# Optimization experiments

Measured on AMD Instinct MI355X. Metric: run time of the kernel, lower is better.

Reference implementation:

```python
import jax, jax.numpy as jnp
import numpy as np
import math

N = 50000
E = 500000
IN_C = 128
T_FEAT = 16
OUT_C = 128
EPS = 1e-5
NEG_SLOPE = 0.01


def setup_inputs() -> dict:
    key = jax.random.key(0)
    ks = jax.random.split(key, 10)
    x = jax.random.normal(ks[0], (N, IN_C), dtype=jnp.float32)
    edge_index = jax.random.randint(ks[1], (2, E), 0, N, dtype=jnp.int64)
    edge_weight = jax.random.uniform(ks[2], (E,), dtype=jnp.float32)
    time_diff = jax.random.uniform(ks[3], (1,), dtype=jnp.float32)
    d_in = IN_C + T_FEAT
    morning_freq = jax.random.normal(ks[4], (T_FEAT,), dtype=jnp.float32)
    W_gcn = jax.random.normal(ks[5], (d_in, OUT_C), dtype=jnp.float32) / np.sqrt(d_in)
    b_gcn = jnp.zeros((OUT_C,), dtype=jnp.float32)
    gamma = jnp.ones((OUT_C,), dtype=jnp.float32)
    beta = jnp.zeros((OUT_C,), dtype=jnp.float32)
    W_lin = jax.random.normal(ks[6], (OUT_C, OUT_C), dtype=jnp.float32) / np.sqrt(OUT_C)
    b_lin = jax.random.normal(ks[7], (OUT_C,), dtype=jnp.float32) * 0.01
    return {"x": x, "edge_index": edge_index, "edge_weight": edge_weight,
            "time_diff": time_diff, "morning_freq": morning_freq,
            "W_gcn": W_gcn, "b_gcn": b_gcn, "gamma": gamma, "beta": beta,
            "W_lin": W_lin, "b_lin": b_lin}


def _gcn_conv(h, edge_index, edge_weight):
    # PyG GCNConv aggregation: add self-loops (weight 1), symmetric normalization.
    row, col = edge_index[0], edge_index[1]
    loop = jnp.arange(N, dtype=edge_index.dtype)
    row_f = jnp.concatenate([row, loop])
    col_f = jnp.concatenate([col, loop])
    ew_f = jnp.concatenate([edge_weight, jnp.ones((N,), dtype=h.dtype)])
    deg = jax.ops.segment_sum(ew_f, col_f, num_segments=N)
    dinv = jnp.where(deg > 0, jax.lax.rsqrt(jnp.maximum(deg, 1e-12)), 0.0)
    norm = dinv[row_f] * ew_f * dinv[col_f]                 # [E+N]
    msg = h[row_f] * norm[:, None]                          # gather + scale
    return jax.ops.segment_sum(msg, col_f, num_segments=N)  # scatter-add


def reference(x, edge_index, edge_weight, time_diff, morning_freq,
              W_gcn, b_gcn, gamma, beta, W_lin, b_lin):
    td = time_diff[0]
    # time_segment == 'morning_peak': sin encoding, tiled over all nodes
    enc = jnp.sin(td * morning_freq * math.pi)              # [T]
    enc = jnp.broadcast_to(enc[None, :], (x.shape[0], T_FEAT))
    h = jnp.concatenate([x, enc], axis=1)                   # [N, in+T]
    h = h @ W_gcn                                           # GCN linear transform
    h = _gcn_conv(h, edge_index, edge_weight) + b_gcn       # [N, out]
    # BatchNorm1d (training-mode batch statistics, biased variance)
    mean = jnp.mean(h, axis=0)
    var = jnp.mean(jnp.square(h - mean), axis=0)
    h = gamma * (h - mean) * jax.lax.rsqrt(var + EPS) + beta
    h = jnp.where(h >= 0, h, NEG_SLOPE * h)                 # LeakyReLU
    h = h @ W_lin + b_lin                                   # Linear (dropout=eval identity)
    return h
```

## Files before the change

kernel.cpp:

```cpp
#include <hip/hip_runtime.h>
#include <hip/hip_bf16.h>

#define NN 50000
#define NE 500000
#define C 128
#define NBLK ((NN + 255) / 256)
#define SPB (NN / 8)
#define RB 128
#define RROWS ((SPB + RB - 1) / RB)
#define GB ((NN + 63) / 64)
#define BN_EPS 1e-5f
#define NEG 0.01f
#define WSCALE 16777216.0f
#define WMASK  0xFFFFFFFFFFFULL

typedef __attribute__((ext_vector_type(8))) short bf16x8;
typedef __attribute__((ext_vector_type(4))) float f32x4;

__device__ inline unsigned short f2bf(float f) {
    unsigned int u = __float_as_uint(f);
    unsigned int r = (u + 0x7fffu + ((u >> 16) & 1u)) >> 16;
    return (unsigned short)r;
}
__device__ inline unsigned int pack2(float a, float b) {
    return (unsigned int)f2bf(a) | ((unsigned int)f2bf(b) << 16);
}
__device__ inline float4 bf4_to_f4(uint2 u) {
    float4 r;
    r.x = __uint_as_float(u.x << 16);
    r.y = __uint_as_float(u.x & 0xffff0000u);
    r.z = __uint_as_float(u.y << 16);
    r.w = __uint_as_float(u.y & 0xffff0000u);
    return r;
}

__global__ void zero_kernel(float* __restrict__ p, long n) {
    long i = (long)blockIdx.x * blockDim.x + threadIdx.x;
    long s = (long)gridDim.x * blockDim.x;
    for (; i < n; i += s) p[i] = 0.f;
}

__global__ __launch_bounds__(256) void wprep_kernel(const float* __restrict__ Wg,
                                                    const float* __restrict__ Wl,
                                                    unsigned int* __restrict__ Wgt,
                                                    unsigned int* __restrict__ Wlt) {
    const int t = threadIdx.x;
    const int col = t >> 1;
    const int half = t & 1;
    for (int j = 0; j < 32; j++) {
        int ku = half * 32 + j;
        int k0 = 2 * ku;
        unsigned int g = (unsigned int)((ku >> 2) ^ (col & 15));
        unsigned int slot = (unsigned int)col * 64u + (g << 2) + (unsigned int)(ku & 3);
        Wgt[slot] = pack2(Wg[(size_t)k0 * C + col], Wg[(size_t)(k0 + 1) * C + col]);
        Wlt[slot] = pack2(Wl[(size_t)k0 * C + col], Wl[(size_t)(k0 + 1) * C + col]);
    }
}

__global__ void cvec_kernel(const float* __restrict__ td, const float* __restrict__ mf,
                            const float* __restrict__ Wg, float* __restrict__ cvec) {
    int o = threadIdx.x;
    float t = td[0];
    float acc = 0.f;
#pragma unroll
    for (int j = 0; j < 16; j++) {
        float s = sinf(t * mf[j] * 3.14159265358979323846f);
        acc = fmaf(s, Wg[(128 + j) * C + o], acc);
    }
    cvec[o] = acc;
}

__global__ __launch_bounds__(256) void gemm1_kernel(const float* __restrict__ X,
                                                    const unsigned int* __restrict__ Wt,
                                                    const float* __restrict__ cvec,
                                                    unsigned short* __restrict__ Hb) {
    __shared__ unsigned int wsh[8192];
    const int t = threadIdx.x;
#pragma unroll
    for (int i = 0; i < 8; i++)
        ((uint4*)wsh)[t + i * 256] = ((const uint4*)Wt)[t + i * 256];

    const int lane = t & 63;
    const int wid = t >> 6;
    const int lrow = lane & 15;
    const int kb = lane >> 4;
    const int row = blockIdx.x * 64 + wid * 16 + lrow;
    const float* xrow = X + (size_t)min(row, NN - 1) * C;

    f32x4 acc[8];
#pragma unroll
    for (int n = 0; n < 8; n++) acc[n] = (f32x4){0.f, 0.f, 0.f, 0.f};
    __syncthreads();

#pragma unroll
    for (int ks = 0; ks < 4; ks++) {
        float4 a0 = *(const float4*)(xrow + ks * 32 + kb * 8);
        float4 a1 = *(const float4*)(xrow + ks * 32 + kb * 8 + 4);
        union { unsigned int u[4]; bf16x8 v; } af;
        af.u[0] = pack2(a0.x, a0.y); af.u[1] = pack2(a0.z, a0.w);
        af.u[2] = pack2(a1.x, a1.y); af.u[3] = pack2(a1.z, a1.w);
        const unsigned int gp = (unsigned int)((ks * 4 + kb) ^ lrow);
#pragma unroll
        for (int n = 0; n < 8; n++) {
            int col = n * 16 + lrow;
            union { uint4 q; bf16x8 v; } bfm;
            bfm.q = *(const uint4*)&wsh[col * 64 + gp * 4];
            acc[n] = __builtin_amdgcn_mfma_f32_16x16x32_bf16(af.v, bfm.v, acc[n], 0, 0, 0);
        }
    }
    const int orow = blockIdx.x * 64 + wid * 16 + kb * 4;
#pragma unroll
    for (int n = 0; n < 8; n++) {
        int col = n * 16 + lrow;
        float cv = cvec[col];
#pragma unroll
        for (int i = 0; i < 4; i++) {
            int r = orow + i;
            if (r < NN) Hb[(size_t)r * C + col] = f2bf(acc[n][i] + cv);
        }
    }
}

__global__ void hist_kernel(const int* __restrict__ ei, const float* __restrict__ ew,
                            unsigned long long* __restrict__ hist, int* __restrict__ rank) {
    int e = blockIdx.x * blockDim.x + threadIdx.x;
    if (e < NE) {
        int c = ei[NE + e];
        unsigned long long pack = (1ULL << 44) | (unsigned long long)(ew[e] * WSCALE);
        unsigned long long old = atomicAdd(&hist[c], pack);
        rank[e] = (int)(old >> 44);
    }
}

__global__ __launch_bounds__(256) void scanp1_kernel(const unsigned long long* __restrict__ hist,
                                                     int* __restrict__ rptr,
                                                     int* __restrict__ bsum) {
    __shared__ int s[256];
    const int t = threadIdx.x;
    const int i = blockIdx.x * 256 + t;
    int v = (i < NN) ? (int)(hist[i] >> 44) : 0;
    s[t] = v;
    __syncthreads();
    for (int off = 1; off < 256; off <<= 1) {
        int add = (t >= off) ? s[t - off] : 0;
        __syncthreads();
        s[t] += add;
        __syncthreads();
    }
    if (i < NN) rptr[i] = s[t] - v;
    if (t == 255) bsum[blockIdx.x] = s[255];
}

__global__ __launch_bounds__(256) void scanp2_kernel(const int* __restrict__ bsum,
                                                     int* __restrict__ boff) {
    __shared__ int s[256];
    const int t = threadIdx.x;
    int v = (t < NBLK) ? bsum[t] : 0;
    s[t] = v;
    __syncthreads();
    for (int off = 1; off < 256; off <<= 1) {
        int add = (t >= off) ? s[t - off] : 0;
        __syncthreads();
        s[t] += add;
        __syncthreads();
    }
    if (t < NBLK) boff[t] = s[t] - v;
}

__global__ void scanp3_kernel(int* __restrict__ rptr, const int* __restrict__ boff,
                              const unsigned long long* __restrict__ hist,
                              float* __restrict__ dinv) {
    int i = blockIdx.x * blockDim.x + threadIdx.x;
    if (i < NN) {
        rptr[i] += boff[i >> 8];
        float degw = (float)(hist[i] & WMASK) * (1.0f / WSCALE);
        dinv[i] = rsqrtf(degw + 1.0f);
    }
    if (i == 0) rptr[NN] = NE;
}

__global__ void fill_kernel(const int* __restrict__ ei, const float* __restrict__ ew,
                            const float* __restrict__ dinv, const int* __restrict__ rptr,
                            const int* __restrict__ rank, int2* __restrict__ csr) {
    int e = blockIdx.x * blockDim.x + threadIdx.x;
    if (e >= NE) return;
    int r = ei[e], c = ei[NE + e];
    int slot = rptr[c] + rank[e];
    float w = dinv[r] * ew[e] * dinv[c];
    csr[slot] = make_int2(r, __float_as_int(w));
}

__global__ __launch_bounds__(256) void spmm_kernel(const int* __restrict__ rptr,
                                                   const int2* __restrict__ csr,
                                                   const unsigned short* __restrict__ Hb,
                                                   const float* __restrict__ dinv,
                                                   const float* __restrict__ bg,
                                                   float* __restrict__ OUT,
                                                   float* __restrict__ P) {
    const int nl = threadIdx.x >> 5;
    const int lane = threadIdx.x & 31;
    const int node = blockIdx.x * 8 + nl;
    const int ch = lane * 4;
    int s = rptr[node], e = rptr[node + 1];
    float d = dinv[node];
    float dd = d * d;
    float4 h = bf4_to_f4(*(const uint2*)(Hb + (size_t)node * C + ch));
    float4 acc = make_float4(dd * h.x, dd * h.y, dd * h.z, dd * h.w);
    int j = s;
    for (; j + 2 <= e; j += 2) {
        int2 e0 = csr[j], e1 = csr[j + 1];
        float w0 = __int_as_float(e0.y), w1 = __int_as_float(e1.y);
        float4 v0 = bf4_to_f4(*(const uint2*)(Hb + (size_t)e0.x * C + ch));
        float4 v1 = bf4_to_f4(*(const uint2*)(Hb + (size_t)e1.x * C + ch));
        acc.x = fmaf(v0.x, w0, acc.x); acc.y = fmaf(v0.y, w0, acc.y);
        acc.z = fmaf(v0.z, w0, acc.z); acc.w = fmaf(v0.w, w0, acc.w);
        acc.x = fmaf(v1.x, w1, acc.x); acc.y = fmaf(v1.y, w1, acc.y);
        acc.z = fmaf(v1.z, w1, acc.z); acc.w = fmaf(v1.w, w1, acc.w);
    }
    if (j < e) {
        int2 e0 = csr[j];
        float w0 = __int_as_float(e0.y);
        float4 v0 = bf4_to_f4(*(const uint2*)(Hb + (size_t)e0.x * C + ch));
        acc.x = fmaf(v0.x, w0, acc.x); acc.y = fmaf(v0.y, w0, acc.y);
        acc.z = fmaf(v0.z, w0, acc.z); acc.w = fmaf(v0.w, w0, acc.w);
    }
    float4 b = *(const float4*)(bg + ch);
    acc.x += b.x; acc.y += b.y; acc.z += b.z; acc.w += b.w;
    *(float4*)(OUT + (size_t)node * C + ch) = acc;

    __shared__ __align__(16) float4 sred[2][8][32];
    float4 sq = make_float4(acc.x * acc.x, acc.y * acc.y, acc.z * acc.z, acc.w * acc.w);
    sred[0][nl][lane] = acc;
    sred[1][nl][lane] = sq;
    __syncthreads();
    if (nl == 0) {
        float4 s0 = sred[0][0][lane], q0 = sred[1][0][lane];
#pragma unroll
        for (int k = 1; k < 8; k++) {
            float4 a = sred[0][k][lane];
            float4 q = sred[1][k][lane];
            s0.x += a.x; s0.y += a.y; s0.z += a.z; s0.w += a.w;
            q0.x += q.x; q0.y += q.y; q0.z += q.z; q0.w += q.w;
        }
        float* row = P + (size_t)blockIdx.x * 256;
        *(float4*)(row + ch) = s0;
        *(float4*)(row + 128 + ch) = q0;
    }
}

__global__ __launch_bounds__(256) void reduce1_kernel(const float* __restrict__ P,
                                                      float* __restrict__ P2) {
    const int c = threadIdx.x;
    const int r0 = blockIdx.x * RROWS;
    const int r1 = min(r0 + RROWS, SPB);
    float a0 = 0.f, a1 = 0.f, a2 = 0.f, a3 = 0.f;
    int r = r0;
    for (; r + 4 <= r1; r += 4) {
        a0 += P[(size_t)(r + 0) * 256 + c];
        a1 += P[(size_t)(r + 1) * 256 + c];
        a2 += P[(size_t)(r + 2) * 256 + c];
        a3 += P[(size_t)(r + 3) * 256 + c];
    }
    for (; r < r1; r++) a0 += P[(size_t)r * 256 + c];
    P2[(size_t)blockIdx.x * 256 + c] = (a0 + a1) + (a2 + a3);
}

__global__ void bnparam_kernel(const float* __restrict__ P2,
                               const float* __restrict__ gm, const float* __restrict__ bt,
                               float* __restrict__ sc, float* __restrict__ sh) {
    int c = threadIdx.x;
    float s0 = 0.f, s1 = 0.f, q0 = 0.f, q1 = 0.f;
    for (int k = 0; k < RB; k += 2) {
        s0 += P2[(size_t)k * 256 + c];
        q0 += P2[(size_t)k * 256 + 128 + c];
        s1 += P2[(size_t)(k + 1) * 256 + c];
        q1 += P2[(size_t)(k + 1) * 256 + 128 + c];
    }
    float ssum = s0 + s1, ssq = q0 + q1;
    float mean = ssum / (float)NN;
    float var = ssq / (float)NN - mean * mean;
    var = fmaxf(var, 0.f);
    float r = rsqrtf(var + BN_EPS);
    float s = gm[c] * r;
    sc[c] = s;
    sh[c] = bt[c] - mean * s;
}

__global__ __launch_bounds__(256) void final_kernel(float* __restrict__ OUT,
                                                    const unsigned int* __restrict__ Wt,
                                                    const float* __restrict__ bl,
                                                    const float* __restrict__ sc,
                                                    const float* __restrict__ sh) {
    __shared__ unsigned int wsh[8192];
    const int t = threadIdx.x;
#pragma unroll
    for (int i = 0; i < 8; i++)
        ((uint4*)wsh)[t + i * 256] = ((const uint4*)Wt)[t + i * 256];

    const int lane = t & 63;
    const int wid = t >> 6;
    const int lrow = lane & 15;
    const int kb = lane >> 4;
    const int row = blockIdx.x * 64 + wid * 16 + lrow;
    const float* hrow = OUT + (size_t)min(row, NN - 1) * C;

    f32x4 acc[8];
#pragma unroll
    for (int n = 0; n < 8; n++) acc[n] = (f32x4){0.f, 0.f, 0.f, 0.f};
    __syncthreads();

#pragma unroll
    for (int ks = 0; ks < 4; ks++) {
        const int k0 = ks * 32 + kb * 8;
        float4 v0 = *(const float4*)(hrow + k0);
        float4 v1 = *(const float4*)(hrow + k0 + 4);
        float4 s0 = *(const float4*)(sc + k0);
        float4 s1 = *(const float4*)(sc + k0 + 4);
        float4 h0 = *(const float4*)(sh + k0);
        float4 h1 = *(const float4*)(sh + k0 + 4);
        float a[8];
        a[0] = fmaf(v0.x, s0.x, h0.x); a[1] = fmaf(v0.y, s0.y, h0.y);
        a[2] = fmaf(v0.z, s0.z, h0.z); a[3] = fmaf(v0.w, s0.w, h0.w);
        a[4] = fmaf(v1.x, s1.x, h1.x); a[5] = fmaf(v1.y, s1.y, h1.y);
        a[6] = fmaf(v1.z, s1.z, h1.z); a[7] = fmaf(v1.w, s1.w, h1.w);
#pragma unroll
        for (int i = 0; i < 8; i++) a[i] = a[i] >= 0.f ? a[i] : NEG * a[i];
        union { unsigned int u[4]; bf16x8 v; } af;
        af.u[0] = pack2(a[0], a[1]); af.u[1] = pack2(a[2], a[3]);
        af.u[2] = pack2(a[4], a[5]); af.u[3] = pack2(a[6], a[7]);
        const unsigned int gp = (unsigned int)((ks * 4 + kb) ^ lrow);
#pragma unroll
        for (int n = 0; n < 8; n++) {
            int col = n * 16 + lrow;
            union { uint4 q; bf16x8 v; } bfm;
            bfm.q = *(const uint4*)&wsh[col * 64 + gp * 4];
            acc[n] = __builtin_amdgcn_mfma_f32_16x16x32_bf16(af.v, bfm.v, acc[n], 0, 0, 0);
        }
    }
    const int orow = blockIdx.x * 64 + wid * 16 + kb * 4;
#pragma unroll
    for (int n = 0; n < 8; n++) {
        int col = n * 16 + lrow;
        float blv = bl[col];
#pragma unroll
        for (int i = 0; i < 4; i++) {
            int r = orow + i;
            if (r < NN) OUT[(size_t)r * C + col] = acc[n][i] + blv;
        }
    }
}

extern "C" void kernel_launch(void* const* d_in, const int* in_sizes, int n_in,
                              void* d_out, int out_size, void* d_ws, size_t ws_size,
                              hipStream_t stream) {
    const float* x  = (const float*)d_in[0];
    const int*   ei = (const int*)d_in[1];
    const float* ew = (const float*)d_in[2];
    const float* td = (const float*)d_in[3];
    const float* mf = (const float*)d_in[4];
    const float* Wg = (const float*)d_in[5];
    const float* bg = (const float*)d_in[6];
    const float* gm = (const float*)d_in[7];
    const float* bt = (const float*)d_in[8];
    const float* Wl = (const float*)d_in[9];
    const float* bl = (const float*)d_in[10];
    float* out = (float*)d_out;

    unsigned short* h1b = (unsigned short*)d_ws;
    unsigned long long* hist = (unsigned long long*)(h1b + (size_t)NN * C);
    float* dinv   = (float*)(hist + NN);
    float* cvec   = dinv + NN;
    float* sc     = cvec + C;
    float* sh     = sc + C;
    int*   rptr   = (int*)(sh + C);
    int*   bsum   = rptr + NN + 8;
    int*   boff   = bsum + NBLK;
    int*   rank   = boff + NBLK + 8;
    int2*  csr    = (int2*)(rank + NE);
    float* P      = (float*)(csr + NE);
    float* P2     = P + (size_t)SPB * 256;
    unsigned int* Wgt = (unsigned int*)(P2 + RB * 256);
    unsigned int* Wlt = Wgt + 8192;

    zero_kernel<<<128, 256, 0, stream>>>((float*)hist, 2L * NN);
    wprep_kernel<<<1, 256, 0, stream>>>(Wg, Wl, Wgt, Wlt);
    cvec_kernel<<<1, 128, 0, stream>>>(td, mf, Wg, cvec);
    gemm1_kernel<<<GB, 256, 0, stream>>>(x, Wgt, cvec, h1b);
    hist_kernel<<<(NE + 255) / 256, 256, 0, stream>>>(ei, ew, hist, rank);
    scanp1_kernel<<<NBLK, 256, 0, stream>>>(hist, rptr, bsum);
    scanp2_kernel<<<1, 256, 0, stream>>>(bsum, boff);
    scanp3_kernel<<<NBLK, 256, 0, stream>>>(rptr, boff, hist, dinv);
    fill_kernel<<<(NE + 255) / 256, 256, 0, stream>>>(ei, ew, dinv, rptr, rank, csr);
    spmm_kernel<<<SPB, 256, 0, stream>>>(rptr, csr, h1b, dinv, bg, out, P);
    reduce1_kernel<<<RB, 256, 0, stream>>>(P, P2);
    bnparam_kernel<<<1, 128, 0, stream>>>(P2, gm, bt, sc, sh);
    final_kernel<<<GB, 256, 0, stream>>>(out, Wlt, bl, sc, sh);
}
```

Measured before the change: 147.9 us.

## Fuse small launches, merge histogram into GEMM grid, unroll SpMM gather

```diff
diff --git a/kernel.cpp b/kernel.cpp
--- a/kernel.cpp
+++ b/kernel.cpp
@@ -5,6 +5,7 @@
 #define NE 500000
 #define C 128
 #define NBLK ((NN + 255) / 256)
+#define HISTB ((NE + 255) / 256)
 #define SPB (NN / 8)
 #define RB 128
 #define RROWS ((SPB + RB - 1) / RB)
@@ -34,48 +35,68 @@
     return r;
 }
 
-__global__ void zero_kernel(float* __restrict__ p, long n) {
-    long i = (long)blockIdx.x * blockDim.x + threadIdx.x;
-    long s = (long)gridDim.x * blockDim.x;
-    for (; i < n; i += s) p[i] = 0.f;
-}
-
-__global__ __launch_bounds__(256) void wprep_kernel(const float* __restrict__ Wg,
+__global__ __launch_bounds__(256) void setup_kernel(const float* __restrict__ Wg,
                                                     const float* __restrict__ Wl,
                                                     unsigned int* __restrict__ Wgt,
-                                                    unsigned int* __restrict__ Wlt) {
+                                                    unsigned int* __restrict__ Wlt,
+                                                    const float* __restrict__ td,
+                                                    const float* __restrict__ mf,
+                                                    float* __restrict__ cvec,
+                                                    float* __restrict__ zreg) {
+    const int b = blockIdx.x;
     const int t = threadIdx.x;
-    const int col = t >> 1;
-    const int half = t & 1;
-    for (int j = 0; j < 32; j++) {
-        int ku = half * 32 + j;
-        int k0 = 2 * ku;
-        unsigned int g = (unsigned int)((ku >> 2) ^ (col & 15));
-        unsigned int slot = (unsigned int)col * 64u + (g << 2) + (unsigned int)(ku & 3);
-        Wgt[slot] = pack2(Wg[(size_t)k0 * C + col], Wg[(size_t)(k0 + 1) * C + col]);
-        Wlt[slot] = pack2(Wl[(size_t)k0 * C + col], Wl[(size_t)(k0 + 1) * C + col]);
-    }
-}
-
-__global__ void cvec_kernel(const float* __restrict__ td, const float* __restrict__ mf,
-                            const float* __restrict__ Wg, float* __restrict__ cvec) {
-    int o = threadIdx.x;
-    float t = td[0];
-    float acc = 0.f;
-#pragma unroll
-    for (int j = 0; j < 16; j++) {
-        float s = sinf(t * mf[j] * 3.14159265358979323846f);
-        acc = fmaf(s, Wg[(128 + j) * C + o], acc);
-    }
-    cvec[o] = acc;
-}
-
-__global__ __launch_bounds__(256) void gemm1_kernel(const float* __restrict__ X,
+    if (b < 128) {
+        long i = (long)b * 256 + t;
+        const long n = 2L * NN + 4;
+        const long s = 128L * 256;
+        for (; i < n; i += s) zreg[i] = 0.f;
+    } else if (b == 128) {
+        const int col = t >> 1;
+        const int half = t & 1;
+        for (int j = 0; j < 32; j++) {
+            int ku = half * 32 + j;
+            int k0 = 2 * ku;
+            unsigned int g = (unsigned int)((ku >> 2) ^ (col & 15));
+            unsigned int slot = (unsigned int)col * 64u + (g << 2) + (unsigned int)(ku & 3);
+            Wgt[slot] = pack2(Wg[(size_t)k0 * C + col], Wg[(size_t)(k0 + 1) * C + col]);
+            Wlt[slot] = pack2(Wl[(size_t)k0 * C + col], Wl[(size_t)(k0 + 1) * C + col]);
+        }
+    } else {
+        if (t < 128) {
+            float tv = td[0];
+            float acc = 0.f;
+#pragma unroll
+            for (int j = 0; j < 16; j++) {
+                float s = sinf(tv * mf[j] * 3.14159265358979323846f);
+                acc = fmaf(s, Wg[(128 + j) * C + t], acc);
+            }
+            cvec[t] = acc;
+        }
+    }
+}
+
+__global__ __launch_bounds__(256) void mega1_kernel(const float* __restrict__ X,
                                                     const unsigned int* __restrict__ Wt,
                                                     const float* __restrict__ cvec,
-                                                    unsigned short* __restrict__ Hb) {
+                                                    unsigned short* __restrict__ Hb,
+                                                    const int* __restrict__ ei,
+                                                    const float* __restrict__ ew,
+                                                    unsigned long long* __restrict__ hist,
+                                                    int* __restrict__ rank) {
     __shared__ unsigned int wsh[8192];
+    const int bid = blockIdx.x;
     const int t = threadIdx.x;
+    if (bid < HISTB) {
+        int e = bid * 256 + t;
+        if (e < NE) {
+            int c = ei[NE + e];
+            unsigned long long pack = (1ULL << 44) | (unsigned long long)(ew[e] * WSCALE);
+            unsigned long long old = atomicAdd(&hist[c], pack);
+            rank[e] = (int)(old >> 44);
+        }
+        return;
+    }
+    const int gb = bid - HISTB;
 #pragma unroll
     for (int i = 0; i < 8; i++)
         ((uint4*)wsh)[t + i * 256] = ((const uint4*)Wt)[t + i * 256];
@@ -84,7 +105,7 @@
     const int wid = t >> 6;
     const int lrow = lane & 15;
     const int kb = lane >> 4;
-    const int row = blockIdx.x * 64 + wid * 16 + lrow;
+    const int row = gb * 64 + wid * 16 + lrow;
     const float* xrow = X + (size_t)min(row, NN - 1) * C;
 
     f32x4 acc[8];
@@ -108,7 +129,7 @@
             acc[n] = __builtin_amdgcn_mfma_f32_16x16x32_bf16(af.v, bfm.v, acc[n], 0, 0, 0);
         }
     }
-    const int orow = blockIdx.x * 64 + wid * 16 + kb * 4;
+    const int orow = gb * 64 + wid * 16 + kb * 4;
 #pragma unroll
     for (int n = 0; n < 8; n++) {
         int col = n * 16 + lrow;
@@ -118,17 +139,6 @@
             int r = orow + i;
             if (r < NN) Hb[(size_t)r * C + col] = f2bf(acc[n][i] + cv);
         }
-    }
-}
-
-__global__ void hist_kernel(const int* __restrict__ ei, const float* __restrict__ ew,
-                            unsigned long long* __restrict__ hist, int* __restrict__ rank) {
-    int e = blockIdx.x * blockDim.x + threadIdx.x;
-    if (e < NE) {
-        int c = ei[NE + e];
-        unsigned long long pack = (1ULL << 44) | (unsigned long long)(ew[e] * WSCALE);
-        unsigned long long old = atomicAdd(&hist[c], pack);
-        rank[e] = (int)(old >> 44);
     }
 }
 
@@ -151,32 +161,27 @@
     if (t == 255) bsum[blockIdx.x] = s[255];
 }
 
-__global__ __launch_bounds__(256) void scanp2_kernel(const int* __restrict__ bsum,
-                                                     int* __restrict__ boff) {
-    __shared__ int s[256];
+__global__ __launch_bounds__(256) void scanp3_kernel(int* __restrict__ rptr,
+                                                     const int* __restrict__ bsum,
+                                                     const unsigned long long* __restrict__ hist,
+                                                     float* __restrict__ dinv) {
+    __shared__ int sb[256];
     const int t = threadIdx.x;
-    int v = (t < NBLK) ? bsum[t] : 0;
-    s[t] = v;
-    __syncthreads();
-    for (int off = 1; off < 256; off <<= 1) {
-        int add = (t >= off) ? s[t - off] : 0;
+    const int b = blockIdx.x;
+    sb[t] = (t < NBLK && t < b) ? bsum[t] : 0;
+    __syncthreads();
+    for (int off = 128; off > 0; off >>= 1) {
+        if (t < off) sb[t] += sb[t + off];
         __syncthreads();
-        s[t] += add;
-        __syncthreads();
-    }
-    if (t < NBLK) boff[t] = s[t] - v;
-}
-
-__global__ void scanp3_kernel(int* __restrict__ rptr, const int* __restrict__ boff,
-                              const unsigned long long* __restrict__ hist,
-                              float* __restrict__ dinv) {
-    int i = blockIdx.x * blockDim.x + threadIdx.x;
+    }
+    const int boff = sb[0];
+    const int i = b * 256 + t;
     if (i < NN) {
-        rptr[i] += boff[i >> 8];
+        rptr[i] += boff;
         float degw = (float)(hist[i] & WMASK) * (1.0f / WSCALE);
         dinv[i] = rsqrtf(degw + 1.0f);
     }
-    if (i == 0) rptr[NN] = NE;
+    if (b == 0 && t == 0) rptr[NN] = NE;
 }
 
 __global__ void fill_kernel(const int* __restrict__ ei, const float* __restrict__ ew,
@@ -206,24 +211,34 @@
     float dd = d * d;
     float4 h = bf4_to_f4(*(const uint2*)(Hb + (size_t)node * C + ch));
     float4 acc = make_float4(dd * h.x, dd * h.y, dd * h.z, dd * h.w);
+    float4 accB = make_float4(0.f, 0.f, 0.f, 0.f);
     int j = s;
-    for (; j + 2 <= e; j += 2) {
-        int2 e0 = csr[j], e1 = csr[j + 1];
+    for (; j + 4 <= e; j += 4) {
+        int2 e0 = csr[j], e1 = csr[j + 1], e2 = csr[j + 2], e3 = csr[j + 3];
         float w0 = __int_as_float(e0.y), w1 = __int_as_float(e1.y);
-        float4 v0 = bf4_to_f4(*(const uint2*)(Hb + (size_t)e0.x * C + ch));
-        float4 v1 = bf4_to_f4(*(const uint2*)(Hb + (size_t)e1.x * C + ch));
-        acc.x = fmaf(v0.x, w0, acc.x); acc.y = fmaf(v0.y, w0, acc.y);
-        acc.z = fmaf(v0.z, w0, acc.z); acc.w = fmaf(v0.w, w0, acc.w);
-        acc.x = fmaf(v1.x, w1, acc.x); acc.y = fmaf(v1.y, w1, acc.y);
-        acc.z = fmaf(v1.z, w1, acc.z); acc.w = fmaf(v1.w, w1, acc.w);
-    }
-    if (j < e) {
+        float w2 = __int_as_float(e2.y), w3 = __int_as_float(e3.y);
+        uint2 u0 = *(const uint2*)(Hb + (size_t)e0.x * C + ch);
+        uint2 u1 = *(const uint2*)(Hb + (size_t)e1.x * C + ch);
+        uint2 u2 = *(const uint2*)(Hb + (size_t)e2.x * C + ch);
+        uint2 u3 = *(const uint2*)(Hb + (size_t)e3.x * C + ch);
+        float4 v0 = bf4_to_f4(u0), v1 = bf4_to_f4(u1), v2 = bf4_to_f4(u2), v3 = bf4_to_f4(u3);
+        acc.x = fmaf(v0.x, w0, acc.x);  acc.y = fmaf(v0.y, w0, acc.y);
+        acc.z = fmaf(v0.z, w0, acc.z);  acc.w = fmaf(v0.w, w0, acc.w);
+        accB.x = fmaf(v1.x, w1, accB.x); accB.y = fmaf(v1.y, w1, accB.y);
+        accB.z = fmaf(v1.z, w1, accB.z); accB.w = fmaf(v1.w, w1, accB.w);
+        acc.x = fmaf(v2.x, w2, acc.x);  acc.y = fmaf(v2.y, w2, acc.y);
+        acc.z = fmaf(v2.z, w2, acc.z);  acc.w = fmaf(v2.w, w2, acc.w);
+        accB.x = fmaf(v3.x, w3, accB.x); accB.y = fmaf(v3.y, w3, accB.y);
+        accB.z = fmaf(v3.z, w3, accB.z); accB.w = fmaf(v3.w, w3, accB.w);
+    }
+    for (; j < e; j++) {
         int2 e0 = csr[j];
         float w0 = __int_as_float(e0.y);
         float4 v0 = bf4_to_f4(*(const uint2*)(Hb + (size_t)e0.x * C + ch));
         acc.x = fmaf(v0.x, w0, acc.x); acc.y = fmaf(v0.y, w0, acc.y);
         acc.z = fmaf(v0.z, w0, acc.z); acc.w = fmaf(v0.w, w0, acc.w);
     }
+    acc.x += accB.x; acc.y += accB.y; acc.z += accB.z; acc.w += accB.w;
     float4 b = *(const float4*)(bg + ch);
     acc.x += b.x; acc.y += b.y; acc.z += b.z; acc.w += b.w;
     *(float4*)(OUT + (size_t)node * C + ch) = acc;
@@ -249,7 +264,12 @@
 }
 
 __global__ __launch_bounds__(256) void reduce1_kernel(const float* __restrict__ P,
-                                                      float* __restrict__ P2) {
+                                                      float* __restrict__ P2,
+                                                      unsigned int* __restrict__ cnt,
+                                                      const float* __restrict__ gm,
+                                                      const float* __restrict__ bt,
+                                                      float* __restrict__ sc,
+                                                      float* __restrict__ sh) {
     const int c = threadIdx.x;
     const int r0 = blockIdx.x * RROWS;
     const int r1 = min(r0 + RROWS, SPB);
@@ -263,27 +283,31 @@
     }
     for (; r < r1; r++) a0 += P[(size_t)r * 256 + c];
     P2[(size_t)blockIdx.x * 256 + c] = (a0 + a1) + (a2 + a3);
-}
-
-__global__ void bnparam_kernel(const float* __restrict__ P2,
-                               const float* __restrict__ gm, const float* __restrict__ bt,
-                               float* __restrict__ sc, float* __restrict__ sh) {
-    int c = threadIdx.x;
-    float s0 = 0.f, s1 = 0.f, q0 = 0.f, q1 = 0.f;
-    for (int k = 0; k < RB; k += 2) {
-        s0 += P2[(size_t)k * 256 + c];
-        q0 += P2[(size_t)k * 256 + 128 + c];
-        s1 += P2[(size_t)(k + 1) * 256 + c];
-        q1 += P2[(size_t)(k + 1) * 256 + 128 + c];
-    }
-    float ssum = s0 + s1, ssq = q0 + q1;
-    float mean = ssum / (float)NN;
-    float var = ssq / (float)NN - mean * mean;
-    var = fmaxf(var, 0.f);
-    float r = rsqrtf(var + BN_EPS);
-    float s = gm[c] * r;
-    sc[c] = s;
-    sh[c] = bt[c] - mean * s;
+
+    __threadfence();
+    __shared__ unsigned int done;
+    if (c == 0) done = atomicAdd(cnt, 1u);
+    __syncthreads();
+    if (done == RB - 1) {
+        __threadfence();
+        if (c < 128) {
+            float s0 = 0.f, s1 = 0.f, q0 = 0.f, q1 = 0.f;
+            for (int k = 0; k < RB; k += 2) {
+                s0 += P2[(size_t)k * 256 + c];
+                q0 += P2[(size_t)k * 256 + 128 + c];
+                s1 += P2[(size_t)(k + 1) * 256 + c];
+                q1 += P2[(size_t)(k + 1) * 256 + 128 + c];
+            }
+            float ssum = s0 + s1, ssq = q0 + q1;
+            float mean = ssum / (float)NN;
+            float var = ssq / (float)NN - mean * mean;
+            var = fmaxf(var, 0.f);
+            float rs = rsqrtf(var + BN_EPS);
+            float s = gm[c] * rs;
+            sc[c] = s;
+            sh[c] = bt[c] - mean * s;
+        }
+    }
 }
 
 __global__ __launch_bounds__(256) void final_kernel(float* __restrict__ OUT,
@@ -368,31 +392,26 @@
 
     unsigned short* h1b = (unsigned short*)d_ws;
     unsigned long long* hist = (unsigned long long*)(h1b + (size_t)NN * C);
-    float* dinv   = (float*)(hist + NN);
+    unsigned int* cnt = (unsigned int*)(hist + NN);
+    float* dinv   = (float*)(cnt + 4);
     float* cvec   = dinv + NN;
     float* sc     = cvec + C;
     float* sh     = sc + C;
     int*   rptr   = (int*)(sh + C);
     int*   bsum   = rptr + NN + 8;
-    int*   boff   = bsum + NBLK;
-    int*   rank   = boff + NBLK + 8;
+    int*   rank   = bsum + NBLK + 12;
     int2*  csr    = (int2*)(rank + NE);
     float* P      = (float*)(csr + NE);
     float* P2     = P + (size_t)SPB * 256;
     unsigned int* Wgt = (unsigned int*)(P2 + RB * 256);
     unsigned int* Wlt = Wgt + 8192;
 
-    zero_kernel<<<128, 256, 0, stream>>>((float*)hist, 2L * NN);
-    wprep_kernel<<<1, 256, 0, stream>>>(Wg, Wl, Wgt, Wlt);
-    cvec_kernel<<<1, 128, 0, stream>>>(td, mf, Wg, cvec);
-    gemm1_kernel<<<GB, 256, 0, stream>>>(x, Wgt, cvec, h1b);
-    hist_kernel<<<(NE + 255) / 256, 256, 0, stream>>>(ei, ew, hist, rank);
+    setup_kernel<<<130, 256, 0, stream>>>(Wg, Wl, Wgt, Wlt, td, mf, cvec, (float*)hist);
+    mega1_kernel<<<HISTB + GB, 256, 0, stream>>>(x, Wgt, cvec, h1b, ei, ew, hist, rank);
     scanp1_kernel<<<NBLK, 256, 0, stream>>>(hist, rptr, bsum);
-    scanp2_kernel<<<1, 256, 0, stream>>>(bsum, boff);
-    scanp3_kernel<<<NBLK, 256, 0, stream>>>(rptr, boff, hist, dinv);
-    fill_kernel<<<(NE + 255) / 256, 256, 0, stream>>>(ei, ew, dinv, rptr, rank, csr);
+    scanp3_kernel<<<NBLK, 256, 0, stream>>>(rptr, bsum, hist, dinv);
+    fill_kernel<<<HISTB, 256, 0, stream>>>(ei, ew, dinv, rptr, rank, csr);
     spmm_kernel<<<SPB, 256, 0, stream>>>(rptr, csr, h1b, dinv, bg, out, P);
-    reduce1_kernel<<<RB, 256, 0, stream>>>(P, P2);
-    bnparam_kernel<<<1, 128, 0, stream>>>(P2, gm, bt, sc, sh);
+    reduce1_kernel<<<RB, 256, 0, stream>>>(P, P2, cnt, gm, bt, sc, sh);
     final_kernel<<<GB, 256, 0, stream>>>(out, Wlt, bl, sc, sh);
 }
```

New measurement: 140.1 us. 1.06x faster.
